# Performance work log

Hardware: AMD Instinct MI355X
Metric: run time of the kernel (lower is better)

Reference implementation:

```python
import jax, jax.numpy as jnp
import numpy as np

D, M, K, L, H, BS = 128, 8, 256, 2, 256, 1024


def setup_inputs() -> dict:
    key = jax.random.key(0)
    ks = jax.random.split(key, 7)
    s_d = 1.0 / np.sqrt(D)
    s_2d = 1.0 / np.sqrt(2 * D)
    s_h = 1.0 / np.sqrt(H)
    x = jax.random.normal(ks[0], (BS, D), jnp.float32)
    codebook0 = jax.random.uniform(ks[1], (K, D), jnp.float32, -s_d, s_d)
    codebooks = jax.random.uniform(ks[2], (M - 1, K, D), jnp.float32, -s_d, s_d)
    Wc = jax.random.uniform(ks[3], (M - 1, D, 2 * D), jnp.float32, -s_2d, s_2d)
    bc = jax.random.uniform(ks[4], (M - 1, D), jnp.float32, -s_2d, s_2d)
    W1 = jax.random.uniform(ks[5], (M - 1, L, H, D), jnp.float32, -s_d, s_d)
    W2 = jax.random.uniform(ks[6], (M - 1, L, D, H), jnp.float32, -s_h, s_h)
    return {"x": x, "codebook0": codebook0, "codebooks": codebooks,
            "Wc": Wc, "bc": bc, "W1": W1, "W2": W2}


def _step_targets(xhat, cb, Wc_m, bc_m, W1_m, W2_m):
    """Candidate quantization targets for one step. xhat:[bs,d], cb:[K,d] -> [bs,K,d].
    MLPconcat(concat(zqs, xhat)) is split into the zqs part and the xhat part so the
    [bs*K, 2d] repeat of the torch code is never materialized (same math)."""
    Wz, Wx = Wc_m[:, :D], Wc_m[:, D:]          # Linear(2d,d): y = cc @ W.T + b
    z = cb[None, :, :] + (cb @ Wz.T)[None, :, :] + (xhat @ Wx.T)[:, None, :] + bc_m  # [bs,K,d]
    for l in range(L):
        z = z + jnp.maximum(jnp.einsum('bkd,hd->bkh', z, W1_m[l]), 0.0) @ W2_m[l].T
    return z + xhat[:, None, :]


def _encode(x, codebook0, codebooks, Wc, bc, W1, W2):
    # step 0: plain nearest-centroid assignment (assign_to_codebook)
    d0 = (x * x).sum(-1, keepdims=True) + (codebook0 * codebook0).sum(-1) - 2.0 * x @ codebook0.T
    code0 = jnp.argmin(d0, axis=1)
    xhat = codebook0[code0]
    codes = [code0]
    xn = (x * x).sum(-1, keepdims=True)        # [bs,1]
    for m in range(M - 1):
        z = _step_targets(xhat, codebooks[m], Wc[m], bc[m], W1[m], W2[m])  # [bs,K,d]
        dist = xn + (z * z).sum(-1) - 2.0 * jnp.einsum('bd,bkd->bk', x, z)
        idx = jnp.argmin(dist, axis=1)
        xhat = jnp.take_along_axis(z, idx[:, None, None], axis=1)[:, 0, :]
        codes.append(idx)
    return jnp.stack(codes, axis=1)            # [bs, M] int


def _decode(codes, codebook0, codebooks, Wc, bc, W1, W2):
    xhat = codebook0[codes[:, 0]]
    side = [xhat]
    for m in range(M - 1):
        zq = codebooks[m][codes[:, m + 1]]     # [bs,d]
        Wz, Wx = Wc[m][:, :D], Wc[m][:, D:]
        z = zq + zq @ Wz.T + xhat @ Wx.T + bc[m]
        for l in range(L):
            z = z + jnp.maximum(z @ W1[m, l].T, 0.0) @ W2[m, l].T
        xhat = xhat + z
        side.append(xhat)
    return xhat, side


def reference(x, codebook0, codebooks, Wc, bc, W1, W2):
    # forward(): encode under no_grad, then differentiable decode with side outputs
    codes = jax.lax.stop_gradient(_encode(x, codebook0, codebooks, Wc, bc, W1, W2))
    xhat, side = _decode(codes, codebook0, codebooks, Wc, bc, W1, W2)
    return (xhat, codes, tuple(side))
```

## Files before the change

kernel.cpp:

```cpp
#include <hip/hip_runtime.h>


typedef _Float16 f16;
typedef f16 half4_t __attribute__((ext_vector_type(4)));
typedef f16 half8_t __attribute__((ext_vector_type(8)));
typedef float f32x16 __attribute__((ext_vector_type(16)));

#define OUT_CODES 131072
#define OUT_SIDE  139264

#define WS_XHAT  0
#define WS_RB    131072
#define WS_Y     262144
#define WS_ZC    393216
#define WS_BESTD 425984
#define WS_BESTI 430080
#define WS_BESTZ 434176

__device__ __forceinline__ f32x16 mfma_f16(half8_t a, half8_t b, f32x16 c) {
  return __builtin_amdgcn_mfma_f32_32x32x16_f16(a, b, c, 0, 0, 0);
}

__device__ __forceinline__ void split8s(float4 p, float4 q, half8_t& hi, half8_t& lo) {
  float s[8] = {p.x, p.y, p.z, p.w, q.x, q.y, q.z, q.w};
#pragma unroll
  for (int i = 0; i < 8; i++) {
    float v = s[i] * 256.f;
    f16 h = (f16)v;
    hi[i] = h;
    lo[i] = (f16)(v - (float)h);
  }
}

__device__ __forceinline__ half8_t ldsB(const f16* base, int m, int d0) {
  int rot = (m & 15) << 2;
  const f16* r = base + m * 128;
  half4_t a = *(const half4_t*)(r + ((d0 + rot) & 127));
  half4_t b = *(const half4_t*)(r + ((d0 + 4 + rot) & 127));
  return __builtin_shufflevector(a, b, 0, 1, 2, 3, 4, 5, 6, 7);
}

__global__ __launch_bounds__(256) void k_step0(const float* __restrict__ x,
    const float* __restrict__ cb0, float* __restrict__ ws, float* __restrict__ out)
{
  __shared__ float xs[128];
  __shared__ float redv[4];
  __shared__ int   redi[4];
  __shared__ int   kwin;
  int tx = threadIdx.x, b = blockIdx.x;
  if (tx < 128) xs[tx] = x[b * 128 + tx];
  __syncthreads();
  const float* c = cb0 + tx * 128;
  float s = 0.f;
  for (int d = 0; d < 128; d += 4) {
    float4 cv = *(const float4*)(c + d);
    float4 xv = *(const float4*)(xs + d);
    float a0 = xv.x - cv.x, a1 = xv.y - cv.y, a2 = xv.z - cv.z, a3 = xv.w - cv.w;
    s += a0 * a0 + a1 * a1 + a2 * a2 + a3 * a3;
  }
  float v = s; int idx = tx;
  for (int off = 32; off; off >>= 1) {
    float v2 = __shfl_xor(v, off);
    int   i2 = __shfl_xor(idx, off);
    if (v2 < v || (v2 == v && i2 < idx)) { v = v2; idx = i2; }
  }
  if ((tx & 63) == 0) { redv[tx >> 6] = v; redi[tx >> 6] = idx; }
  __syncthreads();
  if (tx == 0) {
    float bv = redv[0]; int bi = redi[0];
    for (int w = 1; w < 4; w++)
      if (redv[w] < bv || (redv[w] == bv && redi[w] < bi)) { bv = redv[w]; bi = redi[w]; }
    kwin = bi;
    out[OUT_CODES + b * 8] = (float)bi;
  }
  __syncthreads();
  int k = kwin;
  if (tx < 128) {
    float xh = cb0[k * 128 + tx];
    ws[WS_XHAT + b * 128 + tx] = xh;
    ws[WS_RB   + b * 128 + tx] = xs[tx] - xh;
    out[OUT_SIDE + b * 128 + tx] = xh;
  }
}

__global__ __launch_bounds__(128) void k_prep(const float* __restrict__ cb,
    const float* __restrict__ Wc, const float* __restrict__ bcm, float* __restrict__ ws)
{
  __shared__ float row[128];
  int tx = threadIdx.x, blk = blockIdx.x;
  if (blk < 256) {
    row[tx] = cb[blk * 128 + tx];
    __syncthreads();
    const float* wrow = Wc + tx * 256;
    float s = 0.f;
    for (int d = 0; d < 128; d += 4) {
      float4 wv = *(const float4*)(wrow + d);
      float4 zv = *(const float4*)(row + d);
      s += wv.x * zv.x + wv.y * zv.y + wv.z * zv.z + wv.w * zv.w;
    }
    ws[WS_ZC + blk * 128 + tx] = row[tx] + s + bcm[tx];
  } else {
    int b = blk - 256;
    row[tx] = ws[WS_XHAT + b * 128 + tx];
    __syncthreads();
    const float* wrow = Wc + tx * 256 + 128;
    float s = 0.f;
    for (int d = 0; d < 128; d += 4) {
      float4 wv = *(const float4*)(wrow + d);
      float4 zv = *(const float4*)(row + d);
      s += wv.x * zv.x + wv.y * zv.y + wv.z * zv.z + wv.w * zv.w;
    }
    ws[WS_Y + b * 128 + tx] = s;
  }
}

__global__ __launch_bounds__(256, 2) void k_step(const float* __restrict__ W1g,
    const float* __restrict__ W2g, float* __restrict__ ws, int sm)
{
  __shared__ f16 Zh[8192];
  __shared__ f16 Zl[8192];
  __shared__ f16 Hh[8192];
  __shared__ f16 Hl[8192];
  int tx = threadIdx.x;
  int lane = tx & 63, w = tx >> 6;
  int col = lane & 31, koct = lane >> 5;
  int b = blockIdx.x >> 2, t = blockIdx.x & 3, k0 = t << 6;

  {
    const float* zc = ws + WS_ZC + k0 * 128;
    const float* y  = ws + WS_Y + b * 128;
    for (int idx = tx; idx < 1024; idx += 256) {
      int m = idx & 63, d0 = (idx >> 6) << 3;
      float4 a  = *(const float4*)(zc + m * 128 + d0);
      float4 bb = *(const float4*)(zc + m * 128 + d0 + 4);
      float4 ya = *(const float4*)(y + d0);
      float4 yb = *(const float4*)(y + d0 + 4);
      float sv[8] = {a.x + ya.x, a.y + ya.y, a.z + ya.z, a.w + ya.w,
                     bb.x + yb.x, bb.y + yb.y, bb.z + yb.z, bb.w + yb.w};
      int rot = (m & 15) << 2;
      int c0 = (d0 + rot) & 127, c1 = (d0 + 4 + rot) & 127;
      half4_t h0, l0, h1, l1;
#pragma unroll
      for (int j = 0; j < 4; j++) {
        float v = sv[j] * 256.f;
        f16 h = (f16)v; h0[j] = h; l0[j] = (f16)(v - (float)h);
        v = sv[j + 4] * 256.f;
        h = (f16)v; h1[j] = h; l1[j] = (f16)(v - (float)h);
      }
      *(half4_t*)(Zh + m * 128 + c0) = h0;
      *(half4_t*)(Zl + m * 128 + c0) = l0;
      *(half4_t*)(Zh + m * 128 + c1) = h1;
      *(half4_t*)(Zl + m * 128 + c1) = l1;
    }
  }
  __syncthreads();

  for (int l = 0; l < 2; l++) {
    const float* w1l = W1g + (size_t)(sm * 2 + l) * (256 * 128);
    const float* w2l = W2g + (size_t)(sm * 2 + l) * (128 * 256);
    f32x16 acc2[2];
#pragma unroll
    for (int i = 0; i < 16; i++) { acc2[0][i] = 0.f; acc2[1][i] = 0.f; }

#pragma unroll
    for (int hf = 0; hf < 2; hf++) {
      f32x16 acc1[2];
#pragma unroll
      for (int i = 0; i < 16; i++) { acc1[0][i] = 0.f; acc1[1][i] = 0.f; }
      const float* w1base = w1l + (size_t)(hf * 128 + (w << 5) + col) * 128 + (koct << 3);
#pragma unroll
      for (int kc = 0; kc < 8; kc++) {
        int d0 = kc << 4;
        float4 p = *(const float4*)(w1base + d0);
        float4 q = *(const float4*)(w1base + d0 + 4);
        half8_t ah, al; split8s(p, q, ah, al);
        int dd = d0 + (koct << 3);
        half8_t bh0 = ldsB(Zh, col, dd);
        half8_t bl0 = ldsB(Zl, col, dd);
        acc1[0] = mfma_f16(ah, bh0, acc1[0]);
        acc1[0] = mfma_f16(al, bh0, acc1[0]);
        acc1[0] = mfma_f16(ah, bl0, acc1[0]);
        half8_t bh1 = ldsB(Zh, col + 32, dd);
        half8_t bl1 = ldsB(Zl, col + 32, dd);
        acc1[1] = mfma_f16(ah, bh1, acc1[1]);
        acc1[1] = mfma_f16(al, bh1, acc1[1]);
        acc1[1] = mfma_f16(ah, bl1, acc1[1]);
      }
#pragma unroll
      for (int mt = 0; mt < 2; mt++) {
        int mrow = (mt << 5) + col;
        int rot = (mrow & 15) << 2;
        f16* hhr = Hh + mrow * 128;
        f16* hlr = Hl + mrow * 128;
#pragma unroll
        for (int qd = 0; qd < 4; qd++) {
          half4_t hv, lv;
#pragma unroll
          for (int j = 0; j < 4; j++) {
            float tv = fmaxf(acc1[mt][(qd << 2) + j], 0.f) * 0.00390625f;
            f16 h = (f16)tv; hv[j] = h; lv[j] = (f16)(tv - (float)h);
          }
          int c = (((w << 5) + (qd << 3) + (koct << 2)) + rot) & 127;
          *(half4_t*)(hhr + c) = hv;
          *(half4_t*)(hlr + c) = lv;
        }
      }
      __syncthreads();
      const float* w2base = w2l + (size_t)((w << 5) + col) * 256 + hf * 128 + (koct << 3);
#pragma unroll
      for (int kc = 0; kc < 8; kc++) {
        int h0 = kc << 4;
        float4 p = *(const float4*)(w2base + h0);
        float4 q = *(const float4*)(w2base + h0 + 4);
        half8_t ah, al; split8s(p, q, ah, al);
        int hh0 = h0 + (koct << 3);
        half8_t bh0 = ldsB(Hh, col, hh0);
        half8_t bl0 = ldsB(Hl, col, hh0);
        acc2[0] = mfma_f16(ah, bh0, acc2[0]);
        acc2[0] = mfma_f16(al, bh0, acc2[0]);
        acc2[0] = mfma_f16(ah, bl0, acc2[0]);
        half8_t bh1 = ldsB(Hh, col + 32, hh0);
        half8_t bl1 = ldsB(Hl, col + 32, hh0);
        acc2[1] = mfma_f16(ah, bh1, acc2[1]);
        acc2[1] = mfma_f16(al, bh1, acc2[1]);
        acc2[1] = mfma_f16(ah, bl1, acc2[1]);
      }
      __syncthreads();
    }
#pragma unroll
    for (int mt = 0; mt < 2; mt++) {
      int mrow = (mt << 5) + col;
      int rot = (mrow & 15) << 2;
      f16* zhr = Zh + mrow * 128;
      f16* zlr = Zl + mrow * 128;
#pragma unroll
      for (int qd = 0; qd < 4; qd++) {
        int c = (((w << 5) + (qd << 3) + (koct << 2)) + rot) & 127;
        half4_t zh = *(half4_t*)(zhr + c);
        half4_t zl = *(half4_t*)(zlr + c);
#pragma unroll
        for (int j = 0; j < 4; j++) {
          float zs = (float)zh[j] + (float)zl[j];
          zs += acc2[mt][(qd << 2) + j] * 0.00390625f;
          f16 h = (f16)zs; zh[j] = h; zl[j] = (f16)(zs - (float)h);
        }
        *(half4_t*)(zhr + c) = zh;
        *(half4_t*)(zlr + c) = zl;
      }
    }
    __syncthreads();
  }

  float* pd = (float*)Hh;
  int* rwin = (int*)Hh + 64;
  {
    int row = tx >> 2, seg = tx & 3;
    const float* rb = ws + WS_RB + b * 128 + (seg << 5);
    int rot = (row & 15) << 2;
    const f16* zhr = Zh + row * 128;
    const f16* zlr = Zl + row * 128;
    float s = 0.f;
#pragma unroll
    for (int o = 0; o < 4; o++) {
      int d = (seg << 5) + (o << 3);
      int c0 = (d + rot) & 127, c1 = (d + 4 + rot) & 127;
      half4_t zh0 = *(const half4_t*)(zhr + c0);
      half4_t zl0 = *(const half4_t*)(zlr + c0);
      half4_t zh1 = *(const half4_t*)(zhr + c1);
      half4_t zl1 = *(const half4_t*)(zlr + c1);
      float4 r0 = *(const float4*)(rb + (o << 3));
      float4 r1 = *(const float4*)(rb + (o << 3) + 4);
      float z, dlt;
      z = ((float)zh0[0] + (float)zl0[0]) * 0.00390625f; dlt = r0.x - z; s += dlt * dlt;
      z = ((float)zh0[1] + (float)zl0[1]) * 0.00390625f; dlt = r0.y - z; s += dlt * dlt;
      z = ((float)zh0[2] + (float)zl0[2]) * 0.00390625f; dlt = r0.z - z; s += dlt * dlt;
      z = ((float)zh0[3] + (float)zl0[3]) * 0.00390625f; dlt = r0.w - z; s += dlt * dlt;
      z = ((float)zh1[0] + (float)zl1[0]) * 0.00390625f; dlt = r1.x - z; s += dlt * dlt;
      z = ((float)zh1[1] + (float)zl1[1]) * 0.00390625f; dlt = r1.y - z; s += dlt * dlt;
      z = ((float)zh1[2] + (float)zl1[2]) * 0.00390625f; dlt = r1.z - z; s += dlt * dlt;
      z = ((float)zh1[3] + (float)zl1[3]) * 0.00390625f; dlt = r1.w - z; s += dlt * dlt;
    }
    s += __shfl_xor(s, 1);
    s += __shfl_xor(s, 2);
    if (seg == 0) pd[row] = s;
  }
  __syncthreads();
  if (tx < 64) {
    float v = pd[tx]; int idx = tx;
#pragma unroll
    for (int off = 32; off; off >>= 1) {
      float v2 = __shfl_xor(v, off);
      int   i2 = __shfl_xor(idx, off);
      if (v2 < v || (v2 == v && i2 < idx)) { v = v2; idx = i2; }
    }
    if (tx == 0) {
      ws[WS_BESTD + (b << 2) + t] = v;
      ((int*)ws)[WS_BESTI + (b << 2) + t] = k0 + idx;
      rwin[0] = idx;
    }
  }
  __syncthreads();
  if (tx < 32) {
    int rw = rwin[0];
    int c = ((tx << 2) + ((rw & 15) << 2)) & 127;
    half4_t zh = *(const half4_t*)(Zh + rw * 128 + c);
    half4_t zl = *(const half4_t*)(Zl + rw * 128 + c);
    float4 z;
    z.x = ((float)zh[0] + (float)zl[0]) * 0.00390625f;
    z.y = ((float)zh[1] + (float)zl[1]) * 0.00390625f;
    z.z = ((float)zh[2] + (float)zl[2]) * 0.00390625f;
    z.w = ((float)zh[3] + (float)zl[3]) * 0.00390625f;
    *(float4*)(ws + WS_BESTZ + (((b << 2) + t) << 7) + (tx << 2)) = z;
  }
}

__global__ __launch_bounds__(128) void k_update(const float* __restrict__ x,
    float* __restrict__ ws, float* __restrict__ out, int m, int last)
{
  __shared__ int tsel;
  int tx = threadIdx.x, b = blockIdx.x;
  if (tx == 0) {
    float bv = ws[WS_BESTD + (b << 2)]; int bt = 0;
    for (int q = 1; q < 4; q++) {
      float v = ws[WS_BESTD + (b << 2) + q];
      if (v < bv) { bv = v; bt = q; }
    }
    tsel = bt;
    int k = ((const int*)ws)[WS_BESTI + (b << 2) + bt];
    out[OUT_CODES + b * 8 + (m + 1)] = (float)k;
  }
  __syncthreads();
  int bt = tsel;
  float z  = ws[WS_BESTZ + (((b << 2) + bt) << 7) + tx];
  float xh = ws[WS_XHAT + b * 128 + tx] + z;
  ws[WS_XHAT + b * 128 + tx] = xh;
  ws[WS_RB   + b * 128 + tx] = x[b * 128 + tx] - xh;
  out[OUT_SIDE + (m + 1) * 131072 + b * 128 + tx] = xh;
  if (last) out[b * 128 + tx] = xh;
}

extern "C" void kernel_launch(void* const* d_in, const int* in_sizes, int n_in,
                              void* d_out, int out_size, void* d_ws, size_t ws_size,
                              hipStream_t stream)
{
  const float* x   = (const float*)d_in[0];
  const float* cb0 = (const float*)d_in[1];
  const float* cbs = (const float*)d_in[2];
  const float* Wc  = (const float*)d_in[3];
  const float* bc  = (const float*)d_in[4];
  const float* W1  = (const float*)d_in[5];
  const float* W2  = (const float*)d_in[6];
  float* out = (float*)d_out;
  float* ws  = (float*)d_ws;

  k_step0<<<1024, 256, 0, stream>>>(x, cb0, ws, out);
  for (int m = 0; m < 7; m++) {
    k_prep<<<1280, 128, 0, stream>>>(cbs + m * 256 * 128, Wc + m * 128 * 256,
                                     bc + m * 128, ws);
    k_step<<<4096, 256, 0, stream>>>(W1, W2, ws, m);
    k_update<<<1024, 128, 0, stream>>>(x, ws, out, m, (m == 6) ? 1 : 0);
  }
}
```

Measured before the change: 2.355 ms.

## Pre-split MLP weights to f16 hi/lo once and restructure step kernel tiling

A new pre-pass kernel converts W1 and W2 into scaled f16 hi/lo pairs in workspace once per call, so the step kernel loads ready f16 operands instead of splitting fp32 weights in every one of its 4096 blocks. The step kernel now processes the hidden dimension in four 64-wide chunks with a smaller H buffer in shared memory. This reduces LDS use so occupancy can rise from two to three blocks per CU, and the LDS rotation swizzle changes to 8-element granularity for 128-bit accesses. The old kernel is kept as a fallback when the workspace is too small. The cost is an extra launch, more global memory traffic for the split weights, and extra barriers per chunk.

Result: slower. 2.970 ms (+26.1%).

```diff
diff --git a/kernel.cpp b/kernel.cpp
--- a/kernel.cpp
+++ b/kernel.cpp
@@ -16,28 +16,32 @@
 #define WS_BESTD 425984
 #define WS_BESTI 430080
 #define WS_BESTZ 434176
+#define WS_WSPLIT 960000
+#define NW1 458752
+#define WS_NEED_BYTES (WS_WSPLIT * 4 + 4 * NW1 * 2)
 
 __device__ __forceinline__ f32x16 mfma_f16(half8_t a, half8_t b, f32x16 c) {
   return __builtin_amdgcn_mfma_f32_32x32x16_f16(a, b, c, 0, 0, 0);
 }
 
-__device__ __forceinline__ void split8s(float4 p, float4 q, half8_t& hi, half8_t& lo) {
-  float s[8] = {p.x, p.y, p.z, p.w, q.x, q.y, q.z, q.w};
-#pragma unroll
-  for (int i = 0; i < 8; i++) {
-    float v = s[i] * 256.f;
-    f16 h = (f16)v;
-    hi[i] = h;
-    lo[i] = (f16)(v - (float)h);
-  }
-}
-
-__device__ __forceinline__ half8_t ldsB(const f16* base, int m, int d0) {
-  int rot = (m & 15) << 2;
-  const f16* r = base + m * 128;
-  half4_t a = *(const half4_t*)(r + ((d0 + rot) & 127));
-  half4_t b = *(const half4_t*)(r + ((d0 + 4 + rot) & 127));
-  return __builtin_shufflevector(a, b, 0, 1, 2, 3, 4, 5, 6, 7);
+__global__ __launch_bounds__(256) void k_wsplit(const float* __restrict__ W1,
+    const float* __restrict__ W2, f16* __restrict__ wsh)
+{
+  int i = (blockIdx.x * 256 + threadIdx.x) * 4;
+  const float* src;
+  f16* hi;
+  if (i < NW1) { src = W1 + i; hi = wsh + i; }
+  else         { src = W2 + (i - NW1); hi = wsh + 2 * NW1 + (i - NW1); }
+  f16* lo = hi + NW1;
+  float4 v = *(const float4*)src;
+  half4_t h, l;
+  float s;
+  s = v.x * 256.f; h[0] = (f16)s; l[0] = (f16)(s - (float)h[0]);
+  s = v.y * 256.f; h[1] = (f16)s; l[1] = (f16)(s - (float)h[1]);
+  s = v.z * 256.f; h[2] = (f16)s; l[2] = (f16)(s - (float)h[2]);
+  s = v.w * 256.f; h[3] = (f16)s; l[3] = (f16)(s - (float)h[3]);
+  *(half4_t*)hi = h;
+  *(half4_t*)lo = l;
 }
 
 __global__ __launch_bounds__(256) void k_step0(const float* __restrict__ x,
@@ -114,7 +118,206 @@
   }
 }
 
-__global__ __launch_bounds__(256, 2) void k_step(const float* __restrict__ W1g,
+__global__ __launch_bounds__(256, 3) void k_step(const f16* __restrict__ wsh,
+    float* __restrict__ ws, int sm)
+{
+  __shared__ f16 Zh[8192];
+  __shared__ f16 Zl[8192];
+  __shared__ f16 Hh[4096];
+  __shared__ f16 Hl[4096];
+  int tx = threadIdx.x;
+  int lane = tx & 63, w = tx >> 6;
+  int col = lane & 31, koct = lane >> 5;
+  int b = blockIdx.x >> 2, t = blockIdx.x & 3, k0 = t << 6;
+
+  {
+    const float* zc = ws + WS_ZC + k0 * 128;
+    const float* y  = ws + WS_Y + b * 128;
+    for (int idx = tx; idx < 1024; idx += 256) {
+      int m = idx & 63, d0 = (idx >> 6) << 3;
+      float4 a  = *(const float4*)(zc + m * 128 + d0);
+      float4 bb = *(const float4*)(zc + m * 128 + d0 + 4);
+      float4 ya = *(const float4*)(y + d0);
+      float4 yb = *(const float4*)(y + d0 + 4);
+      float sv[8] = {a.x + ya.x, a.y + ya.y, a.z + ya.z, a.w + ya.w,
+                     bb.x + yb.x, bb.y + yb.y, bb.z + yb.z, bb.w + yb.w};
+      half8_t h8, l8;
+#pragma unroll
+      for (int j = 0; j < 8; j++) {
+        float v = sv[j] * 256.f;
+        f16 h = (f16)v; h8[j] = h; l8[j] = (f16)(v - (float)h);
+      }
+      int c0 = (d0 + ((m & 15) << 3)) & 127;
+      *(half8_t*)(Zh + m * 128 + c0) = h8;
+      *(half8_t*)(Zl + m * 128 + c0) = l8;
+    }
+  }
+  __syncthreads();
+
+  int hsub = w >> 1, msub = w & 1;
+  int mA = (msub << 5) + col;
+  int zrot = (mA & 15) << 3;
+  int hrotA = (mA & 7) << 3;
+  int hrotB = (col & 7) << 3;
+
+  for (int l = 0; l < 2; l++) {
+    const f16* w1h = wsh + (size_t)((sm * 2 + l) * 256) * 128;
+    const f16* w2h = wsh + 2 * NW1 + (size_t)((sm * 2 + l) * 128) * 256;
+    f32x16 acc2[2];
+#pragma unroll
+    for (int i = 0; i < 16; i++) { acc2[0][i] = 0.f; acc2[1][i] = 0.f; }
+
+#pragma unroll
+    for (int hq = 0; hq < 4; hq++) {
+      f32x16 acc1;
+#pragma unroll
+      for (int i = 0; i < 16; i++) acc1[i] = 0.f;
+      const f16* a1h = w1h + (size_t)((hq << 6) + (hsub << 5) + col) * 128 + (koct << 3);
+      const f16* a1l = a1h + NW1;
+#pragma unroll
+      for (int kc = 0; kc < 8; kc++) {
+        half8_t ah = *(const half8_t*)(a1h + (kc << 4));
+        half8_t al = *(const half8_t*)(a1l + (kc << 4));
+        int c = (((kc << 4) + (koct << 3)) + zrot) & 127;
+        half8_t bh = *(const half8_t*)(Zh + mA * 128 + c);
+        half8_t bl = *(const half8_t*)(Zl + mA * 128 + c);
+        acc1 = mfma_f16(ah, bh, acc1);
+        acc1 = mfma_f16(al, bh, acc1);
+        acc1 = mfma_f16(ah, bl, acc1);
+      }
+#pragma unroll
+      for (int qd = 0; qd < 4; qd++) {
+        half4_t hv, lv;
+#pragma unroll
+        for (int j = 0; j < 4; j++) {
+          float tv = fmaxf(acc1[(qd << 2) + j], 0.f) * 0.00390625f;
+          f16 h = (f16)tv; hv[j] = h; lv[j] = (f16)(tv - (float)h);
+        }
+        int c = (((hsub << 5) + (qd << 3) + (koct << 2)) + hrotA) & 63;
+        *(half4_t*)(Hh + (mA << 6) + c) = hv;
+        *(half4_t*)(Hl + (mA << 6) + c) = lv;
+      }
+      __syncthreads();
+      const f16* a2h = w2h + (size_t)((w << 5) + col) * 256 + (hq << 6) + (koct << 3);
+      const f16* a2l = a2h + NW1;
+#pragma unroll
+      for (int kc = 0; kc < 4; kc++) {
+        half8_t ah = *(const half8_t*)(a2h + (kc << 4));
+        half8_t al = *(const half8_t*)(a2l + (kc << 4));
+        int c = (((kc << 4) + (koct << 3)) + hrotB) & 63;
+        half8_t bh0 = *(const half8_t*)(Hh + (col << 6) + c);
+        half8_t bl0 = *(const half8_t*)(Hl + (col << 6) + c);
+        acc2[0] = mfma_f16(ah, bh0, acc2[0]);
+        acc2[0] = mfma_f16(al, bh0, acc2[0]);
+        acc2[0] = mfma_f16(ah, bl0, acc2[0]);
+        half8_t bh1 = *(const half8_t*)(Hh + ((col + 32) << 6) + c);
+        half8_t bl1 = *(const half8_t*)(Hl + ((col + 32) << 6) + c);
+        acc2[1] = mfma_f16(ah, bh1, acc2[1]);
+        acc2[1] = mfma_f16(al, bh1, acc2[1]);
+        acc2[1] = mfma_f16(ah, bl1, acc2[1]);
+      }
+      __syncthreads();
+    }
+#pragma unroll
+    for (int mt = 0; mt < 2; mt++) {
+      int m = (mt << 5) + col;
+      int rot = (m & 15) << 3;
+      f16* zhr = Zh + m * 128;
+      f16* zlr = Zl + m * 128;
+#pragma unroll
+      for (int qd = 0; qd < 4; qd++) {
+        int c = (((w << 5) + (qd << 3) + (koct << 2)) + rot) & 127;
+        half4_t zh = *(half4_t*)(zhr + c);
+        half4_t zl = *(half4_t*)(zlr + c);
+#pragma unroll
+        for (int j = 0; j < 4; j++) {
+          float zs = (float)zh[j] + (float)zl[j];
+          zs += acc2[mt][(qd << 2) + j] * 0.00390625f;
+          f16 h = (f16)zs; zh[j] = h; zl[j] = (f16)(zs - (float)h);
+        }
+        *(half4_t*)(zhr + c) = zh;
+        *(half4_t*)(zlr + c) = zl;
+      }
+    }
+    __syncthreads();
+  }
+
+  float* pd = (float*)Hh;
+  int* rwin = (int*)Hh + 64;
+  {
+    int row = tx >> 2, seg = tx & 3;
+    int rot = (row & 15) << 3;
+    const f16* zhr = Zh + row * 128;
+    const f16* zlr = Zl + row * 128;
+    const float* rb = ws + WS_RB + b * 128 + (seg << 5);
+    float s = 0.f;
+#pragma unroll
+    for (int o = 0; o < 4; o++) {
+      int c = (((seg << 5) + (o << 3)) + rot) & 127;
+      half8_t zh = *(const half8_t*)(zhr + c);
+      half8_t zl = *(const half8_t*)(zlr + c);
+      float4 r0 = *(const float4*)(rb + (o << 3));
+      float4 r1 = *(const float4*)(rb + (o << 3) + 4);
+      float rr[8] = {r0.x, r0.y, r0.z, r0.w, r1.x, r1.y, r1.z, r1.w};
+#pragma unroll
+      for (int j = 0; j < 8; j++) {
+        float z = ((float)zh[j] + (float)zl[j]) * 0.00390625f;
+        float dlt = rr[j] - z;
+        s += dlt * dlt;
+      }
+    }
+    s += __shfl_xor(s, 1);
+    s += __shfl_xor(s, 2);
+    if (seg == 0) pd[row] = s;
+  }
+  __syncthreads();
+  if (tx < 64) {
+    float v = pd[tx]; int idx = tx;
+#pragma unroll
+    for (int off = 32; off; off >>= 1) {
+      float v2 = __shfl_xor(v, off);
+      int   i2 = __shfl_xor(idx, off);
+      if (v2 < v || (v2 == v && i2 < idx)) { v = v2; idx = i2; }
+    }
+    if (tx == 0) {
+      ws[WS_BESTD + (b << 2) + t] = v;
+      ((int*)ws)[WS_BESTI + (b << 2) + t] = k0 + idx;
+      rwin[0] = idx;
+    }
+  }
+  __syncthreads();
+  if (tx < 32) {
+    int rw = rwin[0];
+    int c = ((tx << 2) + ((rw & 15) << 3)) & 127;
+    half4_t zh = *(const half4_t*)(Zh + rw * 128 + c);
+    half4_t zl = *(const half4_t*)(Zl + rw * 128 + c);
+    float4 z;
+    z.x = ((float)zh[0] + (float)zl[0]) * 0.00390625f;
+    z.y = ((float)zh[1] + (float)zl[1]) * 0.00390625f;
+    z.z = ((float)zh[2] + (float)zl[2]) * 0.00390625f;
+    z.w = ((float)zh[3] + (float)zl[3]) * 0.00390625f;
+    *(float4*)(ws + WS_BESTZ + (((b << 2) + t) << 7) + (tx << 2)) = z;
+  }
+}
+
+__device__ __forceinline__ void split8s(float4 p, float4 q, half8_t& hi, half8_t& lo) {
+  float s[8] = {p.x, p.y, p.z, p.w, q.x, q.y, q.z, q.w};
+#pragma unroll
+  for (int i = 0; i < 8; i++) {
+    float v = s[i] * 256.f;
+    f16 h = (f16)v;
+    hi[i] = h;
+    lo[i] = (f16)(v - (float)h);
+  }
+}
+__device__ __forceinline__ half8_t ldsB(const f16* base, int m, int d0) {
+  int rot = (m & 15) << 2;
+  const f16* r = base + m * 128;
+  half4_t a = *(const half4_t*)(r + ((d0 + rot) & 127));
+  half4_t b = *(const half4_t*)(r + ((d0 + 4 + rot) & 127));
+  return __builtin_shufflevector(a, b, 0, 1, 2, 3, 4, 5, 6, 7);
+}
+__global__ __launch_bounds__(256, 2) void k_step_fb(const float* __restrict__ W1g,
     const float* __restrict__ W2g, float* __restrict__ ws, int sm)
 {
   __shared__ f16 Zh[8192];
@@ -125,7 +328,6 @@
   int lane = tx & 63, w = tx >> 6;
   int col = lane & 31, koct = lane >> 5;
   int b = blockIdx.x >> 2, t = blockIdx.x & 3, k0 = t << 6;
-
   {
     const float* zc = ws + WS_ZC + k0 * 128;
     const float* y  = ws + WS_Y + b * 128;
@@ -154,14 +356,12 @@
     }
   }
   __syncthreads();
-
   for (int l = 0; l < 2; l++) {
     const float* w1l = W1g + (size_t)(sm * 2 + l) * (256 * 128);
     const float* w2l = W2g + (size_t)(sm * 2 + l) * (128 * 256);
     f32x16 acc2[2];
 #pragma unroll
     for (int i = 0; i < 16; i++) { acc2[0][i] = 0.f; acc2[1][i] = 0.f; }
-
 #pragma unroll
     for (int hf = 0; hf < 2; hf++) {
       f32x16 acc1[2];
@@ -250,7 +450,6 @@
     }
     __syncthreads();
   }
-
   float* pd = (float*)Hh;
   int* rwin = (int*)Hh + 64;
   {
@@ -352,12 +551,16 @@
   const float* W2  = (const float*)d_in[6];
   float* out = (float*)d_out;
   float* ws  = (float*)d_ws;
-
+  f16* wsh = (f16*)(ws + WS_WSPLIT);
+  const bool pre = ws_size >= (size_t)WS_NEED_BYTES;
+
+  if (pre) k_wsplit<<<896, 256, 0, stream>>>(W1, W2, wsh);
   k_step0<<<1024, 256, 0, stream>>>(x, cb0, ws, out);
   for (int m = 0; m < 7; m++) {
     k_prep<<<1280, 128, 0, stream>>>(cbs + m * 256 * 128, Wc + m * 128 * 256,
                                      bc + m * 128, ws);
-    k_step<<<4096, 256, 0, stream>>>(W1, W2, ws, m);
+    if (pre) k_step<<<4096, 256, 0, stream>>>(wsh, ws, m);
+    else     k_step_fb<<<4096, 256, 0, stream>>>(W1, W2, ws, m);
     k_update<<<1024, 128, 0, stream>>>(x, ws, out, m, (m == 6) ? 1 : 0);
   }
 }
```

## Pre-split W1/W2 into fp16 hi/lo once and prefetch into registers

Applied to the files above, without the earlier changes.

Adds a one-time kernel that converts W1 and W2 into scaled fp16 hi/lo pairs in workspace, so each step block loads ready half8 fragments instead of loading fp32 weights and splitting them in every block. All A fragments for a half-tile are preloaded into registers up front, the LDS swizzle is changed to 8-element rotation so B fragments come from single 16-byte reads, and the MFMA issue order is interleaved across the two accumulators. The risks are higher register pressure under the 2-blocks-per-SM launch bound and the cost of the extra preprocessing kernel.

Result: faster. 2.138 ms (-9.2%).

```diff
diff --git a/kernel.cpp b/kernel.cpp
--- a/kernel.cpp
+++ b/kernel.cpp
@@ -16,28 +16,33 @@
 #define WS_BESTD 425984
 #define WS_BESTI 430080
 #define WS_BESTZ 434176
+#define WS_WSPLIT 960000
+#define NW1 458752
+
+#define HLO 8192
 
 __device__ __forceinline__ f32x16 mfma_f16(half8_t a, half8_t b, f32x16 c) {
   return __builtin_amdgcn_mfma_f32_32x32x16_f16(a, b, c, 0, 0, 0);
 }
 
-__device__ __forceinline__ void split8s(float4 p, float4 q, half8_t& hi, half8_t& lo) {
-  float s[8] = {p.x, p.y, p.z, p.w, q.x, q.y, q.z, q.w};
-#pragma unroll
-  for (int i = 0; i < 8; i++) {
-    float v = s[i] * 256.f;
-    f16 h = (f16)v;
-    hi[i] = h;
-    lo[i] = (f16)(v - (float)h);
-  }
-}
-
-__device__ __forceinline__ half8_t ldsB(const f16* base, int m, int d0) {
-  int rot = (m & 15) << 2;
-  const f16* r = base + m * 128;
-  half4_t a = *(const half4_t*)(r + ((d0 + rot) & 127));
-  half4_t b = *(const half4_t*)(r + ((d0 + 4 + rot) & 127));
-  return __builtin_shufflevector(a, b, 0, 1, 2, 3, 4, 5, 6, 7);
+__global__ __launch_bounds__(256) void k_wsplit(const float* __restrict__ W1,
+    const float* __restrict__ W2, f16* __restrict__ wsh)
+{
+  int i = (blockIdx.x * 256 + threadIdx.x) * 4;
+  const float* src;
+  f16* hi;
+  if (i < NW1) { src = W1 + i; hi = wsh + i; }
+  else         { src = W2 + (i - NW1); hi = wsh + 2 * NW1 + (i - NW1); }
+  f16* lo = hi + NW1;
+  float4 v = *(const float4*)src;
+  half4_t h, l;
+  float s;
+  s = v.x * 256.f; h[0] = (f16)s; l[0] = (f16)(s - (float)h[0]);
+  s = v.y * 256.f; h[1] = (f16)s; l[1] = (f16)(s - (float)h[1]);
+  s = v.z * 256.f; h[2] = (f16)s; l[2] = (f16)(s - (float)h[2]);
+  s = v.w * 256.f; h[3] = (f16)s; l[3] = (f16)(s - (float)h[3]);
+  *(half4_t*)hi = h;
+  *(half4_t*)lo = l;
 }
 
 __global__ __launch_bounds__(256) void k_step0(const float* __restrict__ x,
@@ -114,13 +119,14 @@
   }
 }
 
-__global__ __launch_bounds__(256, 2) void k_step(const float* __restrict__ W1g,
-    const float* __restrict__ W2g, float* __restrict__ ws, int sm)
-{
-  __shared__ f16 Zh[8192];
-  __shared__ f16 Zl[8192];
-  __shared__ f16 Hh[8192];
-  __shared__ f16 Hl[8192];
+__global__ __launch_bounds__(256, 2) void k_step(const f16* __restrict__ wsh,
+    float* __restrict__ ws, int sm)
+{
+  __shared__ __align__(16) f16 lds[32768];
+  f16* Zh = lds;
+  f16* Zl = lds + HLO;
+  f16* Hh = lds + 2 * HLO;
+  f16* Hl = lds + 3 * HLO;
   int tx = threadIdx.x;
   int lane = tx & 63, w = tx >> 6;
   int col = lane & 31, koct = lane >> 5;
@@ -137,61 +143,68 @@
       float4 yb = *(const float4*)(y + d0 + 4);
       float sv[8] = {a.x + ya.x, a.y + ya.y, a.z + ya.z, a.w + ya.w,
                      bb.x + yb.x, bb.y + yb.y, bb.z + yb.z, bb.w + yb.w};
-      int rot = (m & 15) << 2;
-      int c0 = (d0 + rot) & 127, c1 = (d0 + 4 + rot) & 127;
-      half4_t h0, l0, h1, l1;
-#pragma unroll
-      for (int j = 0; j < 4; j++) {
+      half8_t h8, l8;
+#pragma unroll
+      for (int j = 0; j < 8; j++) {
         float v = sv[j] * 256.f;
-        f16 h = (f16)v; h0[j] = h; l0[j] = (f16)(v - (float)h);
-        v = sv[j + 4] * 256.f;
-        h = (f16)v; h1[j] = h; l1[j] = (f16)(v - (float)h);
-      }
-      *(half4_t*)(Zh + m * 128 + c0) = h0;
-      *(half4_t*)(Zl + m * 128 + c0) = l0;
-      *(half4_t*)(Zh + m * 128 + c1) = h1;
-      *(half4_t*)(Zl + m * 128 + c1) = l1;
-    }
-  }
-  __syncthreads();
+        f16 h = (f16)v; h8[j] = h; l8[j] = (f16)(v - (float)h);
+      }
+      int c0 = (d0 + ((m & 15) << 3)) & 127;
+      *(half8_t*)(Zh + (m << 7) + c0) = h8;
+      *(half8_t*)(Zl + (m << 7) + c0) = l8;
+    }
+  }
+  __syncthreads();
+
+  const int rot0 = (col & 15) << 3;
+  const f16* Zr0 = Zh + (col << 7);
+  const f16* Zr1 = Zh + ((col + 32) << 7);
+  const f16* Hr0 = Hh + (col << 7);
+  const f16* Hr1 = Hh + ((col + 32) << 7);
 
   for (int l = 0; l < 2; l++) {
-    const float* w1l = W1g + (size_t)(sm * 2 + l) * (256 * 128);
-    const float* w2l = W2g + (size_t)(sm * 2 + l) * (128 * 256);
+    const f16* w1h = wsh + (size_t)((sm * 2 + l) * 256) * 128;
+    const f16* w2h = wsh + 2 * NW1 + (size_t)((sm * 2 + l) * 128) * 256;
     f32x16 acc2[2];
 #pragma unroll
     for (int i = 0; i < 16; i++) { acc2[0][i] = 0.f; acc2[1][i] = 0.f; }
 
 #pragma unroll
     for (int hf = 0; hf < 2; hf++) {
+      const f16* a1p = w1h + (size_t)((hf << 7) + (w << 5) + col) * 128 + (koct << 3);
+      const f16* a2p = w2h + (size_t)((w << 5) + col) * 256 + (hf << 7) + (koct << 3);
+      half8_t a1hv[8], a1lv[8], a2hv[8], a2lv[8];
+#pragma unroll
+      for (int kc = 0; kc < 8; kc++) {
+        a1hv[kc] = *(const half8_t*)(a1p + (kc << 4));
+        a1lv[kc] = *(const half8_t*)(a1p + NW1 + (kc << 4));
+      }
+#pragma unroll
+      for (int kc = 0; kc < 8; kc++) {
+        a2hv[kc] = *(const half8_t*)(a2p + (kc << 4));
+        a2lv[kc] = *(const half8_t*)(a2p + NW1 + (kc << 4));
+      }
+
       f32x16 acc1[2];
 #pragma unroll
       for (int i = 0; i < 16; i++) { acc1[0][i] = 0.f; acc1[1][i] = 0.f; }
-      const float* w1base = w1l + (size_t)(hf * 128 + (w << 5) + col) * 128 + (koct << 3);
 #pragma unroll
       for (int kc = 0; kc < 8; kc++) {
-        int d0 = kc << 4;
-        float4 p = *(const float4*)(w1base + d0);
-        float4 q = *(const float4*)(w1base + d0 + 4);
-        half8_t ah, al; split8s(p, q, ah, al);
-        int dd = d0 + (koct << 3);
-        half8_t bh0 = ldsB(Zh, col, dd);
-        half8_t bl0 = ldsB(Zl, col, dd);
-        acc1[0] = mfma_f16(ah, bh0, acc1[0]);
-        acc1[0] = mfma_f16(al, bh0, acc1[0]);
-        acc1[0] = mfma_f16(ah, bl0, acc1[0]);
-        half8_t bh1 = ldsB(Zh, col + 32, dd);
-        half8_t bl1 = ldsB(Zl, col + 32, dd);
-        acc1[1] = mfma_f16(ah, bh1, acc1[1]);
-        acc1[1] = mfma_f16(al, bh1, acc1[1]);
-        acc1[1] = mfma_f16(ah, bl1, acc1[1]);
+        int poff = (((kc << 4) + (koct << 3)) + rot0) & 127;
+        half8_t bh0 = *(const half8_t*)(Zr0 + poff);
+        half8_t bl0 = *(const half8_t*)(Zr0 + HLO + poff);
+        half8_t bh1 = *(const half8_t*)(Zr1 + poff);
+        half8_t bl1 = *(const half8_t*)(Zr1 + HLO + poff);
+        acc1[0] = mfma_f16(a1hv[kc], bh0, acc1[0]);
+        acc1[1] = mfma_f16(a1hv[kc], bh1, acc1[1]);
+        acc1[0] = mfma_f16(a1lv[kc], bh0, acc1[0]);
+        acc1[1] = mfma_f16(a1lv[kc], bh1, acc1[1]);
+        acc1[0] = mfma_f16(a1hv[kc], bl0, acc1[0]);
+        acc1[1] = mfma_f16(a1hv[kc], bl1, acc1[1]);
       }
 #pragma unroll
       for (int mt = 0; mt < 2; mt++) {
-        int mrow = (mt << 5) + col;
-        int rot = (mrow & 15) << 2;
-        f16* hhr = Hh + mrow * 128;
-        f16* hlr = Hl + mrow * 128;
+        int m = (mt << 5) + col;
 #pragma unroll
         for (int qd = 0; qd < 4; qd++) {
           half4_t hv, lv;
@@ -200,42 +213,36 @@
             float tv = fmaxf(acc1[mt][(qd << 2) + j], 0.f) * 0.00390625f;
             f16 h = (f16)tv; hv[j] = h; lv[j] = (f16)(tv - (float)h);
           }
-          int c = (((w << 5) + (qd << 3) + (koct << 2)) + rot) & 127;
-          *(half4_t*)(hhr + c) = hv;
-          *(half4_t*)(hlr + c) = lv;
+          int c = (((w << 5) + (qd << 3) + (koct << 2)) + rot0) & 127;
+          *(half4_t*)(Hh + (m << 7) + c) = hv;
+          *(half4_t*)(Hl + (m << 7) + c) = lv;
         }
       }
       __syncthreads();
-      const float* w2base = w2l + (size_t)((w << 5) + col) * 256 + hf * 128 + (koct << 3);
 #pragma unroll
       for (int kc = 0; kc < 8; kc++) {
-        int h0 = kc << 4;
-        float4 p = *(const float4*)(w2base + h0);
-        float4 q = *(const float4*)(w2base + h0 + 4);
-        half8_t ah, al; split8s(p, q, ah, al);
-        int hh0 = h0 + (koct << 3);
-        half8_t bh0 = ldsB(Hh, col, hh0);
-        half8_t bl0 = ldsB(Hl, col, hh0);
-        acc2[0] = mfma_f16(ah, bh0, acc2[0]);
-        acc2[0] = mfma_f16(al, bh0, acc2[0]);
-        acc2[0] = mfma_f16(ah, bl0, acc2[0]);
-        half8_t bh1 = ldsB(Hh, col + 32, hh0);
-        half8_t bl1 = ldsB(Hl, col + 32, hh0);
-        acc2[1] = mfma_f16(ah, bh1, acc2[1]);
-        acc2[1] = mfma_f16(al, bh1, acc2[1]);
-        acc2[1] = mfma_f16(ah, bl1, acc2[1]);
+        int poff = (((kc << 4) + (koct << 3)) + rot0) & 127;
+        half8_t bh0 = *(const half8_t*)(Hr0 + poff);
+        half8_t bl0 = *(const half8_t*)(Hr0 + HLO + poff);
+        half8_t bh1 = *(const half8_t*)(Hr1 + poff);
+        half8_t bl1 = *(const half8_t*)(Hr1 + HLO + poff);
+        acc2[0] = mfma_f16(a2hv[kc], bh0, acc2[0]);
+        acc2[1] = mfma_f16(a2hv[kc], bh1, acc2[1]);
+        acc2[0] = mfma_f16(a2lv[kc], bh0, acc2[0]);
+        acc2[1] = mfma_f16(a2lv[kc], bh1, acc2[1]);
+        acc2[0] = mfma_f16(a2hv[kc], bl0, acc2[0]);
+        acc2[1] = mfma_f16(a2hv[kc], bl1, acc2[1]);
       }
       __syncthreads();
     }
 #pragma unroll
     for (int mt = 0; mt < 2; mt++) {
-      int mrow = (mt << 5) + col;
-      int rot = (mrow & 15) << 2;
-      f16* zhr = Zh + mrow * 128;
-      f16* zlr = Zl + mrow * 128;
+      int m = (mt << 5) + col;
+      f16* zhr = Zh + (m << 7);
+      f16* zlr = Zl + (m << 7);
 #pragma unroll
       for (int qd = 0; qd < 4; qd++) {
-        int c = (((w << 5) + (qd << 3) + (koct << 2)) + rot) & 127;
+        int c = (((w << 5) + (qd << 3) + (koct << 2)) + rot0) & 127;
         half4_t zh = *(half4_t*)(zhr + c);
         half4_t zl = *(half4_t*)(zlr + c);
 #pragma unroll
@@ -255,30 +262,25 @@
   int* rwin = (int*)Hh + 64;
   {
     int row = tx >> 2, seg = tx & 3;
+    int rotr = (row & 15) << 3;
+    const f16* zhr = Zh + (row << 7);
+    const f16* zlr = Zl + (row << 7);
     const float* rb = ws + WS_RB + b * 128 + (seg << 5);
-    int rot = (row & 15) << 2;
-    const f16* zhr = Zh + row * 128;
-    const f16* zlr = Zl + row * 128;
     float s = 0.f;
 #pragma unroll
     for (int o = 0; o < 4; o++) {
-      int d = (seg << 5) + (o << 3);
-      int c0 = (d + rot) & 127, c1 = (d + 4 + rot) & 127;
-      half4_t zh0 = *(const half4_t*)(zhr + c0);
-      half4_t zl0 = *(const half4_t*)(zlr + c0);
-      half4_t zh1 = *(const half4_t*)(zhr + c1);
-      half4_t zl1 = *(const half4_t*)(zlr + c1);
+      int c = (((seg << 5) + (o << 3)) + rotr) & 127;
+      half8_t zh = *(const half8_t*)(zhr + c);
+      half8_t zl = *(const half8_t*)(zlr + c);
       float4 r0 = *(const float4*)(rb + (o << 3));
       float4 r1 = *(const float4*)(rb + (o << 3) + 4);
-      float z, dlt;
-      z = ((float)zh0[0] + (float)zl0[0]) * 0.00390625f; dlt = r0.x - z; s += dlt * dlt;
-      z = ((float)zh0[1] + (float)zl0[1]) * 0.00390625f; dlt = r0.y - z; s += dlt * dlt;
-      z = ((float)zh0[2] + (float)zl0[2]) * 0.00390625f; dlt = r0.z - z; s += dlt * dlt;
-      z = ((float)zh0[3] + (float)zl0[3]) * 0.00390625f; dlt = r0.w - z; s += dlt * dlt;
-      z = ((float)zh1[0] + (float)zl1[0]) * 0.00390625f; dlt = r1.x - z; s += dlt * dlt;
-      z = ((float)zh1[1] + (float)zl1[1]) * 0.00390625f; dlt = r1.y - z; s += dlt * dlt;
-      z = ((float)zh1[2] + (float)zl1[2]) * 0.00390625f; dlt = r1.z - z; s += dlt * dlt;
-      z = ((float)zh1[3] + (float)zl1[3]) * 0.00390625f; dlt = r1.w - z; s += dlt * dlt;
+      float rr[8] = {r0.x, r0.y, r0.z, r0.w, r1.x, r1.y, r1.z, r1.w};
+#pragma unroll
+      for (int j = 0; j < 8; j++) {
+        float z = ((float)zh[j] + (float)zl[j]) * 0.00390625f;
+        float dlt = rr[j] - z;
+        s += dlt * dlt;
+      }
     }
     s += __shfl_xor(s, 1);
     s += __shfl_xor(s, 2);
@@ -302,9 +304,9 @@
   __syncthreads();
   if (tx < 32) {
     int rw = rwin[0];
-    int c = ((tx << 2) + ((rw & 15) << 2)) & 127;
-    half4_t zh = *(const half4_t*)(Zh + rw * 128 + c);
-    half4_t zl = *(const half4_t*)(Zl + rw * 128 + c);
+    int c = ((tx << 2) + ((rw & 15) << 3)) & 127;
+    half4_t zh = *(const half4_t*)(Zh + (rw << 7) + c);
+    half4_t zl = *(const half4_t*)(Zl + (rw << 7) + c);
     float4 z;
     z.x = ((float)zh[0] + (float)zl[0]) * 0.00390625f;
     z.y = ((float)zh[1] + (float)zl[1]) * 0.00390625f;
@@ -352,12 +354,14 @@
   const float* W2  = (const float*)d_in[6];
   float* out = (float*)d_out;
   float* ws  = (float*)d_ws;
-
+  f16* wsh = (f16*)(ws + WS_WSPLIT);
+
+  k_wsplit<<<896, 256, 0, stream>>>(W1, W2, wsh);
   k_step0<<<1024, 256, 0, stream>>>(x, cb0, ws, out);
   for (int m = 0; m < 7; m++) {
     k_prep<<<1280, 128, 0, stream>>>(cbs + m * 256 * 128, Wc + m * 128 * 256,
                                      bc + m * 128, ws);
-    k_step<<<4096, 256, 0, stream>>>(W1, W2, ws, m);
+    k_step<<<4096, 256, 0, stream>>>(wsh, ws, m);
     k_update<<<1024, 128, 0, stream>>>(x, ws, out, m, (m == 6) ? 1 : 0);
   }
 }
```
